# Kernel tuning notes

Hardware: AMD Instinct MI355X
Metric: run time of the kernel (lower is better)

Reference implementation:

```python
import jax, jax.numpy as jnp
import numpy as np

M = 3.96875  # 127/32: clamp bound of the 8-bit-ish fixed-point format


def fix_x(x, m=M):
    # STE quantize: floor(x*32)/32 in forward, identity grad; then exact clamp to [-m, m]
    x = x * 32
    pos = jax.nn.relu(x)
    pos = pos - jax.lax.stop_gradient(pos) + jnp.floor(pos)
    neg = jax.nn.relu(-x)
    neg = neg - jax.lax.stop_gradient(neg) + jnp.ceil(neg)
    x = (pos - neg) / 32
    pos = m - jax.nn.relu(m - jax.nn.relu(x))
    neg = m - jax.nn.relu(m - jax.nn.relu(-x))
    return pos - neg


def setup_inputs() -> dict:
    key = jax.random.key(0)
    k1, k2, k3 = jax.random.split(key, 3)
    B, OUT, IN = 32, 1024, 1024
    x = jax.random.normal(k1, (B, OUT, IN), dtype=jnp.float32)
    weight = jax.random.normal(k2, (OUT, IN), dtype=jnp.float32) * 0.05
    bias = jax.random.normal(k3, (OUT,), dtype=jnp.float32) * 0.05
    return {"x": x, "weight": weight, "bias": bias}


def reference(x, weight, bias):
    # elementwise product then fake-quant: [B, OUT, IN]
    x = fix_x(x * weight)
    dim3 = x.shape[2]
    # Serial (non-associative) quantized suffix reduction along last axis:
    # acc <- fix_x(x[..., k] + acc) for k = dim3-2 ... 0, acc init = x[..., -1].
    init = x[:, :, -1]                                   # [B, OUT]
    xs = jnp.moveaxis(x[:, :, : dim3 - 1], -1, 0)[::-1]  # [IN-1, B, OUT]

    def step(carry, s):
        return fix_x(s + carry), None

    acc, _ = jax.lax.scan(step, init, xs)                # [B, OUT]
    out = fix_x(acc[:, None, :])                         # [B, 1, OUT]
    out = fix_x(out + bias)
    return out
```

## Files before the change

kernel.cpp:

```cpp
#include <hip/hip_runtime.h>
#include <math.h>


#define IN_DIM  1024
#define OUT_DIM 1024
#define B_DIM   32

typedef float vfloat4 __attribute__((ext_vector_type(4)));

__global__ __launch_bounds__(256) void ffl_kernel(
    const float* __restrict__ x,
    const float* __restrict__ w,
    const float* __restrict__ bias,
    float* __restrict__ out)
{
    const int lane = threadIdx.x & 63;
    const int wid  = threadIdx.x >> 6;

    const int xcd = blockIdx.x & 7;
    const int j   = blockIdx.x >> 3;
    const int o   = (xcd << 7) | (j >> 5);
    const int b   = j & 31;

    const size_t rowx = ((size_t)b * OUT_DIM + o) * IN_DIM;
    const size_t roww = (size_t)o * IN_DIM;
    const int    off  = (wid << 8) + (lane << 2);

    vfloat4 xv = *(const vfloat4*)(x + rowx + off);
    vfloat4 wv = *(const vfloat4*)(w + roww + off);

    int rs = 0;
    int rL = -(1 << 28);
    int rU =  (1 << 28);

    float pe[4] = { xv.x * wv.x, xv.y * wv.y, xv.z * wv.z, xv.w * wv.w };
    #pragma unroll
    for (int e = 0; e < 4; ++e) {
        float t = floorf(pe[e] * 32.0f);
        t = fminf(fmaxf(t, -127.0f), 127.0f);
        int v = (int)t;
        bool isInit = (wid == 3) && (lane == 63) && (e == 3);
        int sE = isInit ? 0 : v;
        int LE = isInit ? v : -127;
        int UE = isInit ? v : 127;
        int ns = sE + rs;
        int nL = min(max(LE + rs, rL), rU);
        int nU = min(max(UE + rs, rL), rU);
        rs = ns; rL = nL; rU = nU;
    }

    #pragma unroll
    for (int m = 1; m < 64; m <<= 1) {
        int ps = __shfl_xor(rs, m, 64);
        int pL = __shfl_xor(rL, m, 64);
        int pU = __shfl_xor(rU, m, 64);
        bool lower = ((lane & m) == 0);
        int sG = lower ? rs : ps;
        int LG = lower ? rL : pL;
        int UG = lower ? rU : pU;
        int sF = lower ? ps : rs;
        int LF = lower ? pL : rL;
        int UF = lower ? pU : rU;
        rs = sF + sG;
        rL = min(max(LF + sG, LG), UG);
        rU = min(max(UF + sG, LG), UG);
    }

    __shared__ int Ss[4], Sl[4], Su[4];
    if (lane == 0) { Ss[wid] = rs; Sl[wid] = rL; Su[wid] = rU; }
    __syncthreads();

    if (threadIdx.x == 0) {
        int cs = Ss[3], cL = Sl[3], cU = Su[3];
        #pragma unroll
        for (int k = 2; k >= 0; --k) {
            int sG = Ss[k], LG = Sl[k], UG = Su[k];
            int nL = min(max(cL + sG, LG), UG);
            int nU = min(max(cU + sG, LG), UG);
            cs = cs + sG; cL = nL; cU = nU;
        }
        float acc = (float)cL * 0.03125f;
        float tb  = acc + bias[o];
        float r   = floorf(tb * 32.0f);
        r = fminf(fmaxf(r, -127.0f), 127.0f);
        out[(size_t)b * OUT_DIM + o] = r * 0.03125f;
    }
}

extern "C" void kernel_launch(void* const* d_in, const int* in_sizes, int n_in,
                              void* d_out, int out_size, void* d_ws, size_t ws_size,
                              hipStream_t stream) {
    const float* x    = (const float*)d_in[0];
    const float* w    = (const float*)d_in[1];
    const float* bias = (const float*)d_in[2];
    float* out = (float*)d_out;

    const int blocks = B_DIM * OUT_DIM;
    ffl_kernel<<<blocks, 256, 0, stream>>>(x, w, bias, out);
}
```

Measured before the change: 194.4 us.

## Process one output row per wavefront instead of per block, in float arithmetic

Each wavefront now handles a full 1024-element row (16 elements per lane, four vector loads each for x and w), so a block covers four batch rows and the launch uses a quarter as many blocks. This removes the shared-memory cross-wave combine and the __syncthreads. The clamp-composition scan now runs in float instead of int, which avoids int/float conversions. More work per lane raises register use and serial latency per lane, while the kernel is bound by reading x from memory.

```diff
diff --git a/kernel.cpp b/kernel.cpp
--- a/kernel.cpp
+++ b/kernel.cpp
@@ -19,67 +19,61 @@
 
     const int xcd = blockIdx.x & 7;
     const int j   = blockIdx.x >> 3;
-    const int o   = (xcd << 7) | (j >> 5);
-    const int b   = j & 31;
+    const int o   = (xcd << 7) | (j >> 3);
+    const int b   = ((j & 7) << 2) | wid;
 
-    const size_t rowx = ((size_t)b * OUT_DIM + o) * IN_DIM;
+    const size_t rowx = ((size_t)b * OUT_DIM + o) * (size_t)IN_DIM;
     const size_t roww = (size_t)o * IN_DIM;
-    const int    off  = (wid << 8) + (lane << 2);
+    const int    base = lane << 4;
 
-    vfloat4 xv = *(const vfloat4*)(x + rowx + off);
-    vfloat4 wv = *(const vfloat4*)(w + roww + off);
+    vfloat4 xv[4], wv[4];
+    #pragma unroll
+    for (int c = 0; c < 4; ++c)
+        xv[c] = *(const vfloat4*)(x + rowx + base + (c << 2));
+    #pragma unroll
+    for (int c = 0; c < 4; ++c)
+        wv[c] = *(const vfloat4*)(w + roww + base + (c << 2));
 
-    int rs = 0;
-    int rL = -(1 << 28);
-    int rU =  (1 << 28);
+    float rs = 0.0f;
+    float rL = -268435456.0f;
+    float rU =  268435456.0f;
 
-    float pe[4] = { xv.x * wv.x, xv.y * wv.y, xv.z * wv.z, xv.w * wv.w };
     #pragma unroll
-    for (int e = 0; e < 4; ++e) {
-        float t = floorf(pe[e] * 32.0f);
-        t = fminf(fmaxf(t, -127.0f), 127.0f);
-        int v = (int)t;
-        bool isInit = (wid == 3) && (lane == 63) && (e == 3);
-        int sE = isInit ? 0 : v;
-        int LE = isInit ? v : -127;
-        int UE = isInit ? v : 127;
-        int ns = sE + rs;
-        int nL = min(max(LE + rs, rL), rU);
-        int nU = min(max(UE + rs, rL), rU);
-        rs = ns; rL = nL; rU = nU;
+    for (int c = 0; c < 4; ++c) {
+        float px[4] = { xv[c].x * wv[c].x, xv[c].y * wv[c].y,
+                        xv[c].z * wv[c].z, xv[c].w * wv[c].w };
+        #pragma unroll
+        for (int k = 0; k < 4; ++k) {
+            float t = floorf(px[k] * 32.0f);
+            t = fminf(fmaxf(t, -127.0f), 127.0f);
+            const bool isInit = (c == 3) && (k == 3) && (lane == 63);
+            float sE = isInit ? 0.0f : t;
+            float LE = isInit ? t : -127.0f;
+            float UE = isInit ? t : 127.0f;
+            float nL = fminf(fmaxf(LE + rs, rL), rU);
+            float nU = fminf(fmaxf(UE + rs, rL), rU);
+            rs += sE; rL = nL; rU = nU;
+        }
     }
 
     #pragma unroll
     for (int m = 1; m < 64; m <<= 1) {
-        int ps = __shfl_xor(rs, m, 64);
-        int pL = __shfl_xor(rL, m, 64);
-        int pU = __shfl_xor(rU, m, 64);
-        bool lower = ((lane & m) == 0);
-        int sG = lower ? rs : ps;
-        int LG = lower ? rL : pL;
-        int UG = lower ? rU : pU;
-        int sF = lower ? ps : rs;
-        int LF = lower ? pL : rL;
-        int UF = lower ? pU : rU;
-        rs = sF + sG;
-        rL = min(max(LF + sG, LG), UG);
-        rU = min(max(UF + sG, LG), UG);
+        float ps = __shfl_xor(rs, m, 64);
+        float pL = __shfl_xor(rL, m, 64);
+        float pU = __shfl_xor(rU, m, 64);
+        const bool lower = ((lane & m) == 0);
+        float sG = lower ? rs : ps;
+        float LG = lower ? rL : pL;
+        float UG = lower ? rU : pU;
+        float LF = lower ? pL : rL;
+        float UF = lower ? pU : rU;
+        rs = rs + ps;
+        rL = fminf(fmaxf(LF + sG, LG), UG);
+        rU = fminf(fmaxf(UF + sG, LG), UG);
     }
 
-    __shared__ int Ss[4], Sl[4], Su[4];
-    if (lane == 0) { Ss[wid] = rs; Sl[wid] = rL; Su[wid] = rU; }
-    __syncthreads();
-
-    if (threadIdx.x == 0) {
-        int cs = Ss[3], cL = Sl[3], cU = Su[3];
-        #pragma unroll
-        for (int k = 2; k >= 0; --k) {
-            int sG = Ss[k], LG = Sl[k], UG = Su[k];
-            int nL = min(max(cL + sG, LG), UG);
-            int nU = min(max(cU + sG, LG), UG);
-            cs = cs + sG; cL = nL; cU = nU;
-        }
-        float acc = (float)cL * 0.03125f;
+    if (lane == 0) {
+        float acc = rL * 0.03125f;
         float tb  = acc + bias[o];
         float r   = floorf(tb * 32.0f);
         r = fminf(fmaxf(r, -127.0f), 127.0f);
@@ -95,6 +89,6 @@
     const float* bias = (const float*)d_in[2];
     float* out = (float*)d_out;
 
-    const int blocks = B_DIM * OUT_DIM;
+    const int blocks = (B_DIM * OUT_DIM) / 4;
     ffl_kernel<<<blocks, 256, 0, stream>>>(x, w, bias, out);
 }
```

New measurement: 195.3 us (median of 2 runs). Within noise of the previous version (+0.5%).
